# Performance work log

Hardware: AMD Instinct MI355X
Metric: run time of the kernel (lower is better)

## Reference

```python
import jax, jax.numpy as jnp
import numpy as np

ALPHA = 0.2  # LeakyReLU negative slope
MASK_FILL = -9e15


def setup_inputs() -> dict:
    key = jax.random.key(0)
    k1, k2, k3, k4 = jax.random.split(key, 4)
    N, F_IN, F_OUT = 8192, 128, 64
    x = jax.random.normal(k1, (N, F_IN), dtype=jnp.float32)
    adj = jax.random.randint(k2, (N, N), 0, 2, dtype=jnp.int32)
    # xavier_uniform with gain=1.414 (approx sqrt(2))
    gain = 1.414
    lim_w = gain * np.sqrt(6.0 / (F_IN + F_OUT))
    W = jax.random.uniform(k3, (F_IN, F_OUT), minval=-lim_w, maxval=lim_w, dtype=jnp.float32)
    lim_a = gain * np.sqrt(6.0 / (2 * F_OUT + 1))
    a = jax.random.uniform(k4, (2 * F_OUT, 1), minval=-lim_a, maxval=lim_a, dtype=jnp.float32)
    return {"x": x, "adj": adj, "W": W, "a": a}


def reference(x, adj, W, a):
    # h: [N, F_out]
    h = x @ W
    f_out = h.shape[1]
    # Decompose a^T [h_i || h_j] = h_i . a1 + h_j . a2 (exactly the same math,
    # avoids materializing the N*N*2F concat tensor).
    a1 = a[:f_out, 0]  # [F_out]
    a2 = a[f_out:, 0]  # [F_out]
    e = (h @ a1)[:, None] + (h @ a2)[None, :]  # [N, N]
    e = jax.nn.leaky_relu(e, negative_slope=ALPHA)
    e = jnp.where(adj > 0, e, MASK_FILL)
    attention = jax.nn.softmax(e, axis=1)  # row-wise softmax
    h_prime = attention @ h  # [N, F_out]
    return jax.nn.elu(h_prime)  # concat=True branch
```

## Files before the change

kernel.cpp:

```cpp
#include <hip/hip_runtime.h>
#include <math.h>

#define NN 8192
#define FIN 128
#define FOUT 64
#define LRELU 0.2f
#define JSPLIT 16
#define JCH (NN / JSPLIT)
#define HTSTR 520
#define L2E 1.44269504f

typedef _Float16 f16x8 __attribute__((ext_vector_type(8)));
typedef float f32x4 __attribute__((ext_vector_type(4)));
typedef int i32x4 __attribute__((ext_vector_type(4)));

#define WS_HT 0
#define WS_S1 262144
#define WS_S2 270336
#define WS_S2MAX 278528
#define WS_PACC 278544
#define WS_LP (WS_PACC + JSPLIT * NN * FOUT)

__global__ __launch_bounds__(256) void k_hs(const float* __restrict__ x,
                                            const float* __restrict__ W,
                                            const float* __restrict__ a,
                                            float* ws) {
  __shared__ float Wl[FIN * FOUT];
  __shared__ float xl[16 * FIN];
  __shared__ float hl[16 * FOUT];
  const int t = threadIdx.x;
  const int i0 = blockIdx.x * 16;

#pragma unroll
  for (int c = 0; c < 8; ++c) {
    const int flat = c * 1024 + t * 4;
    *(float4*)&Wl[flat] = *(const float4*)&W[flat];
  }
#pragma unroll
  for (int c = 0; c < 2; ++c) {
    const int flat = c * 1024 + t * 4;
    *(float4*)&xl[flat] = *(const float4*)&x[(size_t)i0 * FIN + flat];
  }
  __syncthreads();

  const int r = t >> 4;
  const int fg = t & 15;
  float4 acc = make_float4(0.f, 0.f, 0.f, 0.f);
#pragma unroll 4
  for (int k = 0; k < FIN; ++k) {
    const float xv = xl[r * FIN + k];
    const float4 wv = *(const float4*)&Wl[k * FOUT + fg * 4];
    acc.x = fmaf(xv, wv.x, acc.x);
    acc.y = fmaf(xv, wv.y, acc.y);
    acc.z = fmaf(xv, wv.z, acc.z);
    acc.w = fmaf(xv, wv.w, acc.w);
  }

  float v1 = acc.x * a[fg * 4] + acc.y * a[fg * 4 + 1] +
             acc.z * a[fg * 4 + 2] + acc.w * a[fg * 4 + 3];
  float v2 = acc.x * a[FOUT + fg * 4] + acc.y * a[FOUT + fg * 4 + 1] +
             acc.z * a[FOUT + fg * 4 + 2] + acc.w * a[FOUT + fg * 4 + 3];
  v1 += __shfl_xor(v1, 1); v2 += __shfl_xor(v2, 1);
  v1 += __shfl_xor(v1, 2); v2 += __shfl_xor(v2, 2);
  v1 += __shfl_xor(v1, 4); v2 += __shfl_xor(v2, 4);
  v1 += __shfl_xor(v1, 8); v2 += __shfl_xor(v2, 8);
  if (fg == 0) {
    ws[WS_S1 + i0 + r] = v1;
    ws[WS_S2 + i0 + r] = v2;
  }

  *(float4*)&hl[r * FOUT + fg * 4] = acc;
  __syncthreads();
  _Float16* ht = (_Float16*)(ws + WS_HT);
  if (t < 128) {
    const int f = t >> 1;
    const int off = (t & 1) * 8;
    f16x8 tmp;
#pragma unroll
    for (int u = 0; u < 8; ++u) tmp[u] = (_Float16)hl[(off + u) * FOUT + f];
    *(f16x8*)&ht[(size_t)f * NN + i0 + off] = tmp;
  }
}

__global__ __launch_bounds__(256) void k_s2max(float* ws) {
  __shared__ float red[256];
  const int t = threadIdx.x;
  float v = -1e30f;
#pragma unroll
  for (int i = 0; i < NN / 256; ++i) v = fmaxf(v, ws[WS_S2 + i * 256 + t]);
  red[t] = v;
  __syncthreads();
  for (int s = 128; s >= 1; s >>= 1) {
    if (t < s) red[t] = fmaxf(red[t], red[t + s]);
    __syncthreads();
  }
  if (t == 0) ws[WS_S2MAX] = red[0];
}

__global__ __launch_bounds__(256, 2) void k_main(const int* __restrict__ adj,
                                                 float* ws) {
  __shared__ __align__(16) _Float16 htl[FOUT * HTSTR];
  __shared__ float s2l[JCH];

  const int t = threadIdx.x;
  const int ib = blockIdx.x >> 4;
  const int js = blockIdx.x & 15;
  const int i0 = ib * 64;
  const int jc0 = js * JCH;

  const _Float16* ht = (const _Float16*)(ws + WS_HT);

#pragma unroll
  for (int c = 0; c < 16; ++c) {
    const int chunk = c * 256 + t;
    const int f = chunk >> 6;
    const int off = (chunk & 63) * 8;
    *(f16x8*)&htl[f * HTSTR + off] = *(const f16x8*)&ht[(size_t)f * NN + jc0 + off];
  }
  s2l[t] = ws[WS_S2 + jc0 + t];
  s2l[t + 256] = ws[WS_S2 + jc0 + t + 256];

  const int w = t >> 6;
  const int l = t & 63;
  const int m16 = l & 15;
  const int q8 = (l >> 4) * 8;
  const int row = i0 + w * 16 + m16;

  const float s2max = ws[WS_S2MAX];
  const float s1v = ws[WS_S1 + row];
  const float tmp0 = s1v + s2max;
  const float mv = fmaxf(tmp0, LRELU * tmp0);
  const float mneg = -mv * L2E;

  const int* arow = adj + (size_t)row * NN + jc0 + q8;

  __syncthreads();

  i32x4 av[32];
#pragma unroll
  for (int u = 0; u < 32; ++u)
    av[u] = __builtin_nontemporal_load(
        (const i32x4*)(arow + (u >> 1) * 32 + (u & 1) * 4));

  f32x4 acc[4];
#pragma unroll
  for (int nf = 0; nf < 4; ++nf) acc[nf] = (f32x4){0.f, 0.f, 0.f, 0.f};
  float lacc = 0.f;

#pragma unroll
  for (int it = 0; it < JCH / 32; ++it) {
    const i32x4 a0 = av[2 * it];
    const i32x4 a1 = av[2 * it + 1];
    const float4 s20 = *(const float4*)&s2l[it * 32 + q8];
    const float4 s21 = *(const float4*)&s2l[it * 32 + q8 + 4];

    float e, p[8];
    e = s1v + s20.x; e = fmaxf(e, LRELU * e); p[0] = a0.x ? exp2f(fmaf(e, L2E, mneg)) : 0.f;
    e = s1v + s20.y; e = fmaxf(e, LRELU * e); p[1] = a0.y ? exp2f(fmaf(e, L2E, mneg)) : 0.f;
    e = s1v + s20.z; e = fmaxf(e, LRELU * e); p[2] = a0.z ? exp2f(fmaf(e, L2E, mneg)) : 0.f;
    e = s1v + s20.w; e = fmaxf(e, LRELU * e); p[3] = a0.w ? exp2f(fmaf(e, L2E, mneg)) : 0.f;
    e = s1v + s21.x; e = fmaxf(e, LRELU * e); p[4] = a1.x ? exp2f(fmaf(e, L2E, mneg)) : 0.f;
    e = s1v + s21.y; e = fmaxf(e, LRELU * e); p[5] = a1.y ? exp2f(fmaf(e, L2E, mneg)) : 0.f;
    e = s1v + s21.z; e = fmaxf(e, LRELU * e); p[6] = a1.z ? exp2f(fmaf(e, L2E, mneg)) : 0.f;
    e = s1v + s21.w; e = fmaxf(e, LRELU * e); p[7] = a1.w ? exp2f(fmaf(e, L2E, mneg)) : 0.f;

    f16x8 af;
#pragma unroll
    for (int u = 0; u < 8; ++u) af[u] = (_Float16)p[u];
#pragma unroll
    for (int u = 0; u < 8; ++u) lacc += (float)af[u];

    const int kb = it * 32 + q8;
#pragma unroll
    for (int nf = 0; nf < 4; ++nf) {
      const f16x8 b = *(const f16x8*)&htl[(nf * 16 + m16) * HTSTR + kb];
      acc[nf] = __builtin_amdgcn_mfma_f32_16x16x32_f16(af, b, acc[nf], 0, 0, 0);
    }
  }

  lacc += __shfl_xor(lacc, 16);
  lacc += __shfl_xor(lacc, 32);
  if (l < 16) ws[WS_LP + js * NN + row] = lacc;

  float* pacc = ws + WS_PACC + (size_t)js * (NN * FOUT);
  const int orow = i0 + w * 16 + (l >> 4) * 4;
#pragma unroll
  for (int nf = 0; nf < 4; ++nf)
#pragma unroll
    for (int r = 0; r < 4; ++r)
      __builtin_nontemporal_store(
          acc[nf][r], &pacc[(size_t)(orow + r) * FOUT + nf * 16 + m16]);
}

__global__ __launch_bounds__(256) void k_combine(const float* __restrict__ ws,
                                                 float* __restrict__ out) {
  const int idx = blockIdx.x * 256 + threadIdx.x;
  const int i = idx >> 6;
  float s = 0.f, l = 0.f;
#pragma unroll
  for (int js = 0; js < JSPLIT; ++js) {
    s += ws[WS_PACC + (size_t)js * (NN * FOUT) + idx];
    l += ws[WS_LP + js * NN + i];
  }
  const float v = s / l;
  out[idx] = v > 0.f ? v : expm1f(v);
}

extern "C" void kernel_launch(void* const* d_in, const int* in_sizes, int n_in,
                              void* d_out, int out_size, void* d_ws,
                              size_t ws_size, hipStream_t stream) {
  const float* x = (const float*)d_in[0];
  const int* adj = (const int*)d_in[1];
  const float* W = (const float*)d_in[2];
  const float* a = (const float*)d_in[3];
  float* ws = (float*)d_ws;
  float* out = (float*)d_out;

  hipLaunchKernelGGL(k_hs, dim3(NN / 16), dim3(256), 0, stream, x, W, a, ws);
  hipLaunchKernelGGL(k_s2max, dim3(1), dim3(256), 0, stream, ws);
  hipLaunchKernelGGL(k_main, dim3((NN / 64) * JSPLIT), dim3(256), 0, stream,
                     adj, ws);
  hipLaunchKernelGGL(k_combine, dim3(NN * FOUT / 256), dim3(256), 0, stream,
                     ws, out);
}
```

Measured before the change: 382.2 us.

## Load adjacency rows coalesced and stage probabilities through LDS for MFMA

Each wave now reads whole adjacency row segments with fully coalesced 16-byte loads (lanes span contiguous columns) instead of the strided MFMA-fragment pattern. It computes the exp weights in that layout and writes them as fp16 into a new shared-memory tile, then reloads them in MFMA A-fragment order after a barrier. The s2 values now come from registers instead of shared memory. The extra ~66KB of LDS forces occupancy down to one block per CU (launch bounds changed to 256,1), which risks less latency hiding in this memory-bound kernel.

```diff
diff --git a/kernel.cpp b/kernel.cpp
--- a/kernel.cpp
+++ b/kernel.cpp
@@ -8,9 +8,11 @@
 #define JSPLIT 16
 #define JCH (NN / JSPLIT)
 #define HTSTR 520
+#define PSTRH 520
 #define L2E 1.44269504f
 
 typedef _Float16 f16x8 __attribute__((ext_vector_type(8)));
+typedef _Float16 f16x4 __attribute__((ext_vector_type(4)));
 typedef float f32x4 __attribute__((ext_vector_type(4)));
 typedef int i32x4 __attribute__((ext_vector_type(4)));
 
@@ -97,10 +99,10 @@
   if (t == 0) ws[WS_S2MAX] = red[0];
 }
 
-__global__ __launch_bounds__(256, 2) void k_main(const int* __restrict__ adj,
+__global__ __launch_bounds__(256, 1) void k_main(const int* __restrict__ adj,
                                                  float* ws) {
+  __shared__ __align__(16) _Float16 pal[64 * PSTRH];
   __shared__ __align__(16) _Float16 htl[FOUT * HTSTR];
-  __shared__ float s2l[JCH];
 
   const int t = threadIdx.x;
   const int ib = blockIdx.x >> 4;
@@ -117,31 +119,54 @@
     const int off = (chunk & 63) * 8;
     *(f16x8*)&htl[f * HTSTR + off] = *(const f16x8*)&ht[(size_t)f * NN + jc0 + off];
   }
-  s2l[t] = ws[WS_S2 + jc0 + t];
-  s2l[t + 256] = ws[WS_S2 + jc0 + t + 256];
 
   const int w = t >> 6;
   const int l = t & 63;
   const int m16 = l & 15;
+  const int r0 = w * 16;
+
+  const float s2max = ws[WS_S2MAX];
+  const float sv1 = ws[WS_S1 + i0 + r0 + m16];
+  const float4 s2a = *(const float4*)&ws[WS_S2 + jc0 + l * 4];
+  const float4 s2b = *(const float4*)&ws[WS_S2 + jc0 + 256 + l * 4];
+
+  const int* abase = adj + (size_t)(i0 + r0) * NN + jc0 + l * 4;
+  i32x4 av[32];
+#pragma unroll
+  for (int r = 0; r < 16; ++r) {
+#pragma unroll
+    for (int g = 0; g < 2; ++g)
+      av[r * 2 + g] = __builtin_nontemporal_load(
+          (const i32x4*)(abase + (size_t)r * NN + g * 256));
+  }
+
+#pragma unroll
+  for (int r = 0; r < 16; ++r) {
+    const float s1r = __shfl(sv1, r);
+    const float tm = s1r + s2max;
+    const float mr = fmaxf(tm, LRELU * tm);
+    const float mneg = -mr * L2E;
+#pragma unroll
+    for (int g = 0; g < 2; ++g) {
+      const i32x4 a = av[r * 2 + g];
+      const float4 s2v = g ? s2b : s2a;
+      float e;
+      e = s1r + s2v.x; e = fmaxf(e, LRELU * e);
+      const _Float16 q0 = a.x ? (_Float16)exp2f(fmaf(e, L2E, mneg)) : (_Float16)0.f;
+      e = s1r + s2v.y; e = fmaxf(e, LRELU * e);
+      const _Float16 q1 = a.y ? (_Float16)exp2f(fmaf(e, L2E, mneg)) : (_Float16)0.f;
+      e = s1r + s2v.z; e = fmaxf(e, LRELU * e);
+      const _Float16 q2 = a.z ? (_Float16)exp2f(fmaf(e, L2E, mneg)) : (_Float16)0.f;
+      e = s1r + s2v.w; e = fmaxf(e, LRELU * e);
+      const _Float16 q3 = a.w ? (_Float16)exp2f(fmaf(e, L2E, mneg)) : (_Float16)0.f;
+      f16x4 pv = {q0, q1, q2, q3};
+      *(f16x4*)&pal[(r0 + r) * PSTRH + g * 256 + l * 4] = pv;
+    }
+  }
+
+  __syncthreads();
+
   const int q8 = (l >> 4) * 8;
-  const int row = i0 + w * 16 + m16;
-
-  const float s2max = ws[WS_S2MAX];
-  const float s1v = ws[WS_S1 + row];
-  const float tmp0 = s1v + s2max;
-  const float mv = fmaxf(tmp0, LRELU * tmp0);
-  const float mneg = -mv * L2E;
-
-  const int* arow = adj + (size_t)row * NN + jc0 + q8;
-
-  __syncthreads();
-
-  i32x4 av[32];
-#pragma unroll
-  for (int u = 0; u < 32; ++u)
-    av[u] = __builtin_nontemporal_load(
-        (const i32x4*)(arow + (u >> 1) * 32 + (u & 1) * 4));
-
   f32x4 acc[4];
 #pragma unroll
   for (int nf = 0; nf < 4; ++nf) acc[nf] = (f32x4){0.f, 0.f, 0.f, 0.f};
@@ -149,28 +174,10 @@
 
 #pragma unroll
   for (int it = 0; it < JCH / 32; ++it) {
-    const i32x4 a0 = av[2 * it];
-    const i32x4 a1 = av[2 * it + 1];
-    const float4 s20 = *(const float4*)&s2l[it * 32 + q8];
-    const float4 s21 = *(const float4*)&s2l[it * 32 + q8 + 4];
-
-    float e, p[8];
-    e = s1v + s20.x; e = fmaxf(e, LRELU * e); p[0] = a0.x ? exp2f(fmaf(e, L2E, mneg)) : 0.f;
-    e = s1v + s20.y; e = fmaxf(e, LRELU * e); p[1] = a0.y ? exp2f(fmaf(e, L2E, mneg)) : 0.f;
-    e = s1v + s20.z; e = fmaxf(e, LRELU * e); p[2] = a0.z ? exp2f(fmaf(e, L2E, mneg)) : 0.f;
-    e = s1v + s20.w; e = fmaxf(e, LRELU * e); p[3] = a0.w ? exp2f(fmaf(e, L2E, mneg)) : 0.f;
-    e = s1v + s21.x; e = fmaxf(e, LRELU * e); p[4] = a1.x ? exp2f(fmaf(e, L2E, mneg)) : 0.f;
-    e = s1v + s21.y; e = fmaxf(e, LRELU * e); p[5] = a1.y ? exp2f(fmaf(e, L2E, mneg)) : 0.f;
-    e = s1v + s21.z; e = fmaxf(e, LRELU * e); p[6] = a1.z ? exp2f(fmaf(e, L2E, mneg)) : 0.f;
-    e = s1v + s21.w; e = fmaxf(e, LRELU * e); p[7] = a1.w ? exp2f(fmaf(e, L2E, mneg)) : 0.f;
-
-    f16x8 af;
-#pragma unroll
-    for (int u = 0; u < 8; ++u) af[u] = (_Float16)p[u];
+    const int kb = it * 32 + q8;
+    const f16x8 af = *(const f16x8*)&pal[(r0 + m16) * PSTRH + kb];
 #pragma unroll
     for (int u = 0; u < 8; ++u) lacc += (float)af[u];
-
-    const int kb = it * 32 + q8;
 #pragma unroll
     for (int nf = 0; nf < 4; ++nf) {
       const f16x8 b = *(const f16x8*)&htl[(nf * 16 + m16) * HTSTR + kb];
@@ -180,10 +187,10 @@
 
   lacc += __shfl_xor(lacc, 16);
   lacc += __shfl_xor(lacc, 32);
-  if (l < 16) ws[WS_LP + js * NN + row] = lacc;
+  if (l < 16) ws[WS_LP + js * NN + i0 + r0 + m16] = lacc;
 
   float* pacc = ws + WS_PACC + (size_t)js * (NN * FOUT);
-  const int orow = i0 + w * 16 + (l >> 4) * 4;
+  const int orow = i0 + r0 + (l >> 4) * 4;
 #pragma unroll
   for (int nf = 0; nf < 4; ++nf)
 #pragma unroll
```

Measured after the change: 398.3 us. +4.2%, slower.

## Pack adjacency into bitmask in a pre-pass and read bits in main kernel

Applied to the files above, without the earlier changes.

Adds a k_pack kernel that reads the int32 adjacency matrix once and writes a 1-bit-per-entry mask to workspace. The main attention kernel then loads 16 packed words per row chunk instead of 128 int32 values per thread, which cuts its register use and global traffic. The full 256 MB adjacency read still happens, now in a separate kernel launch. This adds one launch and an 8 MB write/read, and it may free registers for better occupancy in k_main.

```diff
diff --git a/kernel.cpp b/kernel.cpp
--- a/kernel.cpp
+++ b/kernel.cpp
@@ -12,7 +12,6 @@
 
 typedef _Float16 f16x8 __attribute__((ext_vector_type(8)));
 typedef float f32x4 __attribute__((ext_vector_type(4)));
-typedef int i32x4 __attribute__((ext_vector_type(4)));
 
 #define WS_HT 0
 #define WS_S1 262144
@@ -20,6 +19,26 @@
 #define WS_S2MAX 278528
 #define WS_PACC 278544
 #define WS_LP (WS_PACC + JSPLIT * NN * FOUT)
+#define WS_PACKED (WS_LP + JSPLIT * NN)
+
+__global__ __launch_bounds__(256) void k_pack(const int* __restrict__ adj,
+                                              float* ws) {
+  const int gid = blockIdx.x * 256 + threadIdx.x;
+  const int* base = adj + (size_t)gid * 32;
+  int4 av[8];
+#pragma unroll
+  for (int k = 0; k < 8; ++k)
+    av[k] = *(const int4*)(base + k * 4);
+  unsigned int word = 0u;
+#pragma unroll
+  for (int k = 0; k < 8; ++k) {
+    word |= (av[k].x > 0 ? 1u : 0u) << (k * 4 + 0);
+    word |= (av[k].y > 0 ? 1u : 0u) << (k * 4 + 1);
+    word |= (av[k].z > 0 ? 1u : 0u) << (k * 4 + 2);
+    word |= (av[k].w > 0 ? 1u : 0u) << (k * 4 + 3);
+  }
+  ((unsigned int*)(ws + WS_PACKED))[gid] = word;
+}
 
 __global__ __launch_bounds__(256) void k_hs(const float* __restrict__ x,
                                             const float* __restrict__ W,
@@ -97,8 +116,7 @@
   if (t == 0) ws[WS_S2MAX] = red[0];
 }
 
-__global__ __launch_bounds__(256, 2) void k_main(const int* __restrict__ adj,
-                                                 float* ws) {
+__global__ __launch_bounds__(256, 2) void k_main(float* ws) {
   __shared__ __align__(16) _Float16 htl[FOUT * HTSTR];
   __shared__ float s2l[JCH];
 
@@ -132,37 +150,38 @@
   const float mv = fmaxf(tmp0, LRELU * tmp0);
   const float mneg = -mv * L2E;
 
-  const int* arow = adj + (size_t)row * NN + jc0 + q8;
-
-  __syncthreads();
-
-  i32x4 av[32];
-#pragma unroll
-  for (int u = 0; u < 32; ++u)
-    av[u] = __builtin_nontemporal_load(
-        (const i32x4*)(arow + (u >> 1) * 32 + (u & 1) * 4));
+  const unsigned int* prow =
+      (const unsigned int*)(ws + WS_PACKED) + (size_t)row * (NN / 32) + js * 16;
+  uint4 wreg[4];
+#pragma unroll
+  for (int c = 0; c < 4; ++c) wreg[c] = *(const uint4*)(prow + c * 4);
 
   f32x4 acc[4];
 #pragma unroll
   for (int nf = 0; nf < 4; ++nf) acc[nf] = (f32x4){0.f, 0.f, 0.f, 0.f};
   float lacc = 0.f;
 
+  __syncthreads();
+
 #pragma unroll
   for (int it = 0; it < JCH / 32; ++it) {
-    const i32x4 a0 = av[2 * it];
-    const i32x4 a1 = av[2 * it + 1];
+    const uint4 wv = wreg[it >> 2];
+    const unsigned int word = ((it & 3) == 0) ? wv.x
+                            : ((it & 3) == 1) ? wv.y
+                            : ((it & 3) == 2) ? wv.z : wv.w;
+    const unsigned int m8 = (word >> q8) & 0xffu;
     const float4 s20 = *(const float4*)&s2l[it * 32 + q8];
     const float4 s21 = *(const float4*)&s2l[it * 32 + q8 + 4];
 
     float e, p[8];
-    e = s1v + s20.x; e = fmaxf(e, LRELU * e); p[0] = a0.x ? exp2f(fmaf(e, L2E, mneg)) : 0.f;
-    e = s1v + s20.y; e = fmaxf(e, LRELU * e); p[1] = a0.y ? exp2f(fmaf(e, L2E, mneg)) : 0.f;
-    e = s1v + s20.z; e = fmaxf(e, LRELU * e); p[2] = a0.z ? exp2f(fmaf(e, L2E, mneg)) : 0.f;
-    e = s1v + s20.w; e = fmaxf(e, LRELU * e); p[3] = a0.w ? exp2f(fmaf(e, L2E, mneg)) : 0.f;
-    e = s1v + s21.x; e = fmaxf(e, LRELU * e); p[4] = a1.x ? exp2f(fmaf(e, L2E, mneg)) : 0.f;
-    e = s1v + s21.y; e = fmaxf(e, LRELU * e); p[5] = a1.y ? exp2f(fmaf(e, L2E, mneg)) : 0.f;
-    e = s1v + s21.z; e = fmaxf(e, LRELU * e); p[6] = a1.z ? exp2f(fmaf(e, L2E, mneg)) : 0.f;
-    e = s1v + s21.w; e = fmaxf(e, LRELU * e); p[7] = a1.w ? exp2f(fmaf(e, L2E, mneg)) : 0.f;
+    e = s1v + s20.x; e = fmaxf(e, LRELU * e); p[0] = (m8 & 1u)   ? exp2f(fmaf(e, L2E, mneg)) : 0.f;
+    e = s1v + s20.y; e = fmaxf(e, LRELU * e); p[1] = (m8 & 2u)   ? exp2f(fmaf(e, L2E, mneg)) : 0.f;
+    e = s1v + s20.z; e = fmaxf(e, LRELU * e); p[2] = (m8 & 4u)   ? exp2f(fmaf(e, L2E, mneg)) : 0.f;
+    e = s1v + s20.w; e = fmaxf(e, LRELU * e); p[3] = (m8 & 8u)   ? exp2f(fmaf(e, L2E, mneg)) : 0.f;
+    e = s1v + s21.x; e = fmaxf(e, LRELU * e); p[4] = (m8 & 16u)  ? exp2f(fmaf(e, L2E, mneg)) : 0.f;
+    e = s1v + s21.y; e = fmaxf(e, LRELU * e); p[5] = (m8 & 32u)  ? exp2f(fmaf(e, L2E, mneg)) : 0.f;
+    e = s1v + s21.z; e = fmaxf(e, LRELU * e); p[6] = (m8 & 64u)  ? exp2f(fmaf(e, L2E, mneg)) : 0.f;
+    e = s1v + s21.w; e = fmaxf(e, LRELU * e); p[7] = (m8 & 128u) ? exp2f(fmaf(e, L2E, mneg)) : 0.f;
 
     f16x8 af;
 #pragma unroll
@@ -216,10 +235,12 @@
   float* ws = (float*)d_ws;
   float* out = (float*)d_out;
 
+  hipLaunchKernelGGL(k_pack, dim3(NN * NN / 32 / 256), dim3(256), 0, stream,
+                     adj, ws);
   hipLaunchKernelGGL(k_hs, dim3(NN / 16), dim3(256), 0, stream, x, W, a, ws);
   hipLaunchKernelGGL(k_s2max, dim3(1), dim3(256), 0, stream, ws);
   hipLaunchKernelGGL(k_main, dim3((NN / 64) * JSPLIT), dim3(256), 0, stream,
-                     adj, ws);
+                     ws);
   hipLaunchKernelGGL(k_combine, dim3(NN * FOUT / 256), dim3(256), 0, stream,
                      ws, out);
 }
```

After: 421.1 us. 10.2% more time.
